# Performance work log

Hardware: AMD Instinct MI355X
Metric: run time of the kernel (lower is better)

The kernel has to match this reference:

```python
import jax, jax.numpy as jnp
import numpy as np

NUM_HEADS = 8
FOCUSING_FACTOR = 3
EPS = 1e-6


def _focus(x, f):
    # focusing: x**f, renormalized to keep the original L2 norm per token
    n = jnp.linalg.norm(x, axis=-1, keepdims=True)
    xp = x ** f
    return xp / jnp.linalg.norm(xp, axis=-1, keepdims=True) * n


def _split_heads(x, h):
    # b n (h c) -> (b h) n c
    b, n, C = x.shape
    return x.reshape(b, n, h, C // h).transpose(0, 2, 1, 3).reshape(b * h, n, C // h)


def setup_inputs() -> dict:
    key = jax.random.key(0)
    ks = jax.random.split(key, 9)
    B, Nq, Nkv, C = 8, 4096, 4096, 512
    query = jax.random.normal(ks[0], (B, Nq, C), jnp.float32)
    key_in = jax.random.normal(ks[1], (B, Nkv, C), jnp.float32)
    value = jax.random.normal(ks[2], (B, Nkv, C), jnp.float32)
    Wq = jax.random.normal(ks[3], (C, C), jnp.float32) * 0.02
    Wk = jax.random.normal(ks[4], (C, C), jnp.float32) * 0.02
    Wv = jax.random.normal(ks[5], (C, C), jnp.float32) * 0.02
    Wp = jax.random.normal(ks[6], (C, C), jnp.float32) * 0.02
    bp = jnp.zeros((C,), jnp.float32)
    scale = jax.random.normal(ks[7], (1, 1, C), jnp.float32) * 0.02
    return {"query": query, "key_in": key_in, "value": value,
            "Wq": Wq, "Wk": Wk, "Wv": Wv, "Wp": Wp, "bp": bp,
            "scale": scale, "H": 64, "W": 64}


def reference(query, key_in, value, Wq, Wk, Wv, Wp, bp, scale, H, W):
    B, N, C = query.shape
    h = NUM_HEADS
    # projections (qkv_bias=False)
    q = jax.nn.relu(query @ Wq) + EPS
    k = jax.nn.relu(key_in @ Wk) + EPS
    v = value @ Wv
    s = jax.nn.softplus(scale)  # [1,1,C]
    q = q / s
    k = k / s
    q = _focus(q, FOCUSING_FACTOR)
    k = _focus(k, FOCUSING_FACTOR)
    q = _split_heads(q, h)  # [(B h), N, c]
    k = _split_heads(k, h)
    v = _split_heads(v, h)
    # z-normalizer: 1 / (q . sum_j k_j)
    z = 1.0 / (jnp.einsum('bic,bc->bi', q, k.sum(axis=1)) + EPS)
    # O(n) kv-aggregation path (i*j*(c+d) > c*d*(i+j) for these shapes)
    kv = jnp.einsum('bjc,bjd->bcd', k, v)
    x = jnp.einsum('bic,bcd,bi->bid', q, kv, z)
    # (b h) n c -> b n (h c)
    x = x.reshape(B, h, N, C // h).transpose(0, 2, 1, 3).reshape(B, N, C)
    # note: dwc(v) feature_map in the original is dead code (never added to x)
    return x @ Wp + bp
```

## Files before the change

### kernel.cpp

```cpp
#include <hip/hip_runtime.h>
#include <hip/hip_bf16.h>
#include <math.h>

typedef __attribute__((ext_vector_type(8))) short short8;
typedef __attribute__((ext_vector_type(4))) float f32x4;

#define MFMA16x16x32(A,B,C) __builtin_amdgcn_mfma_f32_16x16x32_bf16((A),(B),(C),0,0,0)

__device__ __forceinline__ short f2b(float x) {
  __hip_bfloat16 h = __float2bfloat16(x);
  short s; __builtin_memcpy(&s, &h, 2); return s;
}
__device__ __forceinline__ float b2f(short s) {
  __hip_bfloat16 h; __builtin_memcpy(&h, &s, 2); return __bfloat162float(h);
}

__global__ __launch_bounds__(256)
void prep_kernel(const float* __restrict__ Wq, const float* __restrict__ Wk,
                 const float* __restrict__ Wv, const float* __restrict__ Wp,
                 const float* __restrict__ scale,
                 short* __restrict__ wpack, float* __restrict__ spls)
{
  const int b = blockIdx.x;
  const int t = threadIdx.x;
  if (b == 64) {
    for (int i = t; i < 512; i += 256) {
      float x = scale[i];
      spls[i] = (x > 20.f) ? x : log1pf(expf(x));
    }
    return;
  }
  const float* Ws[4] = {Wq, Wk, Wv, Wp};
  const int w = b >> 4, kf16 = b & 15;
  const float* W = Ws[w];
  short* dst = wpack + (size_t)w * (512 * 512);
  __shared__ short lds[32 * 512];
  for (int i = 0; i < 64; ++i) {
    int idx = i * 256 + t;
    int r = idx >> 9, c = idx & 511;
    lds[idx] = f2b(W[(size_t)(kf16 * 32 + r) * 512 + c]);
  }
  __syncthreads();
  for (int s = 0; s < 8; ++s) {
    int slot = s * 256 + t;
    int nf = slot >> 6, l = slot & 63;
    int n = nf * 16 + (l & 15);
    int k0 = 8 * (l >> 4);
    short8 v;
#pragma unroll
    for (int jj = 0; jj < 8; ++jj) v[jj] = lds[(k0 + jj) * 512 + n];
    *(short8*)(dst + ((size_t)(kf16 * 32 + nf) * 64 + l) * 8) = v;
  }
}

template<int MODE>
__global__ __launch_bounds__(512, 2)
void proj_kernel(const void* __restrict__ Xv, const short* __restrict__ wpk,
                 const float* __restrict__ spls, short* __restrict__ outp,
                 const float* __restrict__ bp, float* __restrict__ outf)
{
  __shared__ short tile[64 * 512];
  __shared__ float pnorm[2][8][64];
  __shared__ float facs[64];
  const int t = threadIdx.x;
  const int lane = t & 63;
  const int wid = t >> 6;
  const int g = lane >> 4;
  const int cl = lane & 15;
  const int rb = blockIdx.x << 6;

  {
    const int r = t >> 3;
    const int c8 = t & 7;
    if (MODE < 3) {
      const float* src = (const float*)Xv + (size_t)(rb + r) * 512;
#pragma unroll
      for (int s = 0; s < 8; ++s) {
        int c = s * 64 + c8 * 8;
        f32x4 a0 = *(const f32x4*)(src + c);
        f32x4 a1 = *(const f32x4*)(src + c + 4);
        short8 v;
#pragma unroll
        for (int j = 0; j < 4; ++j) { v[j] = f2b(a0[j]); v[4 + j] = f2b(a1[j]); }
        int byteoff = (r * 1024 + c * 2) ^ ((r & 7) << 4);
        *(short8*)((char*)tile + byteoff) = v;
      }
    } else {
      const short* src = (const short*)Xv + (size_t)(rb + r) * 512;
#pragma unroll
      for (int s = 0; s < 8; ++s) {
        int c = s * 64 + c8 * 8;
        short8 v = *(const short8*)(src + c);
        int byteoff = (r * 1024 + c * 2) ^ ((r & 7) << 4);
        *(short8*)((char*)tile + byteoff) = v;
      }
    }
  }
  __syncthreads();

  f32x4 zero4 = {0.f, 0.f, 0.f, 0.f};
  f32x4 acc[4][4];
#pragma unroll
  for (int rf = 0; rf < 4; ++rf)
#pragma unroll
    for (int cf = 0; cf < 4; ++cf) acc[rf][cf] = zero4;

  const short8* wp8 = (const short8*)wpk;

  short8 bcur[4], bnxt[4];
#pragma unroll
  for (int cf = 0; cf < 4; ++cf)
    bcur[cf] = wp8[((size_t)(wid * 4 + cf)) * 64 + lane];

  for (int kf = 0; kf < 16; ++kf) {
    if (kf < 15) {
#pragma unroll
      for (int cf = 0; cf < 4; ++cf)
        bnxt[cf] = wp8[((size_t)((kf + 1) * 32 + wid * 4 + cf)) * 64 + lane];
    }
    short8 af[4];
#pragma unroll
    for (int rf = 0; rf < 4; ++rf) {
      int row = rf * 16 + cl;
      int byteoff = (row * 1024 + (kf * 32 + 8 * g) * 2) ^ ((row & 7) << 4);
      af[rf] = *(const short8*)((const char*)tile + byteoff);
    }
#pragma unroll
    for (int rf = 0; rf < 4; ++rf)
#pragma unroll
      for (int cf = 0; cf < 4; ++cf)
        acc[rf][cf] = MFMA16x16x32(af[rf], bcur[cf], acc[rf][cf]);
    if (kf < 15) {
#pragma unroll
      for (int cf = 0; cf < 4; ++cf) bcur[cf] = bnxt[cf];
    }
  }

  if (MODE == 3) {
#pragma unroll
    for (int rf = 0; rf < 4; ++rf)
#pragma unroll
      for (int cf = 0; cf < 4; ++cf) {
        int c = wid * 64 + cf * 16 + cl;
        float bv = bp[c];
#pragma unroll
        for (int j = 0; j < 4; ++j)
          outf[(size_t)(rb + rf * 16 + 4 * g + j) * 512 + c] = acc[rf][cf][j] + bv;
      }
    return;
  }

  if (MODE < 2) {
    float sp_inv[4];
#pragma unroll
    for (int cf = 0; cf < 4; ++cf) sp_inv[cf] = 1.f / spls[wid * 64 + cf * 16 + cl];
    float p2[4][4], p6[4][4];
#pragma unroll
    for (int rf = 0; rf < 4; ++rf)
#pragma unroll
      for (int j = 0; j < 4; ++j) { p2[rf][j] = 0.f; p6[rf][j] = 0.f; }
#pragma unroll
    for (int rf = 0; rf < 4; ++rf)
#pragma unroll
      for (int cf = 0; cf < 4; ++cf)
#pragma unroll
        for (int j = 0; j < 4; ++j) {
          float v = acc[rf][cf][j];
          v = fmaxf(v, 0.f) + 1e-6f;
          v *= sp_inv[cf];
          acc[rf][cf][j] = v;
          float v2 = v * v;
          p2[rf][j] += v2;
          p6[rf][j] += v2 * v2 * v2;
        }
#pragma unroll
    for (int m = 1; m < 16; m <<= 1) {
#pragma unroll
      for (int rf = 0; rf < 4; ++rf)
#pragma unroll
        for (int j = 0; j < 4; ++j) {
          p2[rf][j] += __shfl_xor(p2[rf][j], m, 64);
          p6[rf][j] += __shfl_xor(p6[rf][j], m, 64);
        }
    }
    if (cl == 0) {
#pragma unroll
      for (int rf = 0; rf < 4; ++rf)
#pragma unroll
        for (int j = 0; j < 4; ++j) {
          pnorm[0][wid][rf * 16 + 4 * g + j] = p2[rf][j];
          pnorm[1][wid][rf * 16 + 4 * g + j] = p6[rf][j];
        }
    }
    __syncthreads();
    if (t < 64) {
      float a = 0.f, b = 0.f;
#pragma unroll
      for (int w = 0; w < 8; ++w) { a += pnorm[0][w][t]; b += pnorm[1][w][t]; }
      facs[t] = sqrtf(a / b);
    }
    __syncthreads();
    float fac[4][4];
#pragma unroll
    for (int rf = 0; rf < 4; ++rf)
#pragma unroll
      for (int j = 0; j < 4; ++j) fac[rf][j] = facs[rf * 16 + 4 * g + j];
#pragma unroll
    for (int rf = 0; rf < 4; ++rf)
#pragma unroll
      for (int cf = 0; cf < 4; ++cf)
#pragma unroll
        for (int j = 0; j < 4; ++j) {
          float v = acc[rf][cf][j];
          float o = v * v * v * fac[rf][j];
          int r = rf * 16 + 4 * g + j;
          int c = wid * 64 + cf * 16 + cl;
          int byteoff = (r * 1024 + c * 2) ^ ((r & 7) << 4);
          *(short*)((char*)tile + byteoff) = f2b(o);
        }
  } else {
    __syncthreads();
#pragma unroll
    for (int rf = 0; rf < 4; ++rf)
#pragma unroll
      for (int cf = 0; cf < 4; ++cf)
#pragma unroll
        for (int j = 0; j < 4; ++j) {
          int r = rf * 16 + 4 * g + j;
          int c = wid * 64 + cf * 16 + cl;
          int byteoff = (r * 1024 + c * 2) ^ ((r & 7) << 4);
          *(short*)((char*)tile + byteoff) = f2b(acc[rf][cf][j]);
        }
  }
  __syncthreads();

  if (MODE == 0) {
    const int r = t >> 3;
    const int c8 = t & 7;
#pragma unroll
    for (int s = 0; s < 8; ++s) {
      int ci = c8 + 8 * s;
      int byteoff = (r * 1024 + ci * 16) ^ ((r & 7) << 4);
      short8 v = *(const short8*)((const char*)tile + byteoff);
      *(short8*)(outp + (size_t)(rb + r) * 512 + ci * 8) = v;
    }
  } else {
    const int l = lane;
    const int batch = rb >> 12;
    const int jf_base = (rb & 4095) >> 5;
#pragma unroll
    for (int s = 0; s < 8; ++s) {
      int fidx = wid * 8 + s;
      int jf = fidx >> 5;
      int cf = fidx & 31;
      int c = cf * 16 + (l & 15);
      int j0 = jf * 32 + 8 * (l >> 4);
      short8 v;
#pragma unroll
      for (int jj = 0; jj < 8; ++jj) {
        int j = j0 + jj;
        int byteoff = (j * 1024 + c * 2) ^ ((j & 7) << 4);
        v[jj] = *(const short*)((const char*)tile + byteoff);
      }
      int bh = batch * 8 + (cf >> 2);
      int cfh = cf & 3;
      int jfg = jf_base + jf;
      *(short8*)(outp + (((size_t)(bh * 128 + jfg) * 4 + cfh) * 64 + l) * 8) = v;
    }
  }
}

__global__ __launch_bounds__(256)
void kv_kernel(const short* __restrict__ kpack, const short* __restrict__ vpack,
               float* __restrict__ pKV, float* __restrict__ pKS)
{
  __shared__ float red[4][64 * 64];
  __shared__ float ksacc[64];
  const int t = threadIdx.x;
  const int lane = t & 63;
  const int w = t >> 6;
  const int g = lane >> 4;
  const int cl = lane & 15;
  const int bh = blockIdx.x >> 3;
  const int sp = blockIdx.x & 7;
  if (t < 64) ksacc[t] = 0.f;
  __syncthreads();

  f32x4 zero4 = {0.f, 0.f, 0.f, 0.f};
  f32x4 acc[4][4];
#pragma unroll
  for (int df = 0; df < 4; ++df)
#pragma unroll
    for (int cf = 0; cf < 4; ++cf) acc[df][cf] = zero4;
  float ks[4] = {0.f, 0.f, 0.f, 0.f};
  const short8* kp = (const short8*)kpack;
  const short8* vp = (const short8*)vpack;

#pragma unroll
  for (int i = 0; i < 4; ++i) {
    int jfg = sp * 16 + w * 4 + i;
    size_t base = ((size_t)bh * 128 + jfg) * 4 * 64;
    short8 afr[4], bfr[4];
#pragma unroll
    for (int f = 0; f < 4; ++f) {
      afr[f] = vp[base + (size_t)f * 64 + lane];
      bfr[f] = kp[base + (size_t)f * 64 + lane];
    }
#pragma unroll
    for (int cf = 0; cf < 4; ++cf) {
      float s = 0.f;
#pragma unroll
      for (int jj = 0; jj < 8; ++jj) s += b2f(bfr[cf][jj]);
      ks[cf] += s;
    }
#pragma unroll
    for (int df = 0; df < 4; ++df)
#pragma unroll
      for (int cf = 0; cf < 4; ++cf)
        acc[df][cf] = MFMA16x16x32(afr[df], bfr[cf], acc[df][cf]);
  }

#pragma unroll
  for (int cf = 0; cf < 4; ++cf) {
    ks[cf] += __shfl_xor(ks[cf], 16, 64);
    ks[cf] += __shfl_xor(ks[cf], 32, 64);
  }
  if (lane < 16) {
#pragma unroll
    for (int cf = 0; cf < 4; ++cf) atomicAdd(&ksacc[cf * 16 + lane], ks[cf]);
  }

#pragma unroll
  for (int df = 0; df < 4; ++df)
#pragma unroll
    for (int cf = 0; cf < 4; ++cf)
#pragma unroll
      for (int j = 0; j < 4; ++j)
        red[w][(df * 16 + 4 * g + j) * 64 + cf * 16 + cl] = acc[df][cf][j];
  __syncthreads();

  float* dkv = pKV + (size_t)blockIdx.x * 4096;
  for (int i = t; i < 4096; i += 256)
    dkv[i] = red[0][i] + red[1][i] + red[2][i] + red[3][i];
  if (t < 64) pKS[(size_t)blockIdx.x * 64 + t] = ksacc[t];
}

__global__ __launch_bounds__(256)
void kv_reduce(const float* __restrict__ pKV, const float* __restrict__ pKS,
               short* __restrict__ kvT, float* __restrict__ ksum)
{
  const int bh = blockIdx.x;
  const int t = threadIdx.x;
  for (int i = t; i < 4096; i += 256) {
    float s = 0.f;
#pragma unroll
    for (int sp = 0; sp < 8; ++sp) s += pKV[(size_t)(bh * 8 + sp) * 4096 + i];
    kvT[(size_t)bh * 4096 + i] = f2b(s);
  }
  if (t < 64) {
    float s = 0.f;
#pragma unroll
    for (int sp = 0; sp < 8; ++sp) s += pKS[(size_t)(bh * 8 + sp) * 64 + t];
    ksum[bh * 64 + t] = s;
  }
}

__global__ __launch_bounds__(512)
void x_kernel(const short* __restrict__ qf, const short* __restrict__ kvT,
              const float* __restrict__ ksum, short* __restrict__ xout)
{
  __shared__ short xt[64 * 512];
  __shared__ float ksb[512];
  __shared__ float zb[64 * 8];
  const int t = threadIdx.x;
  const int lane = t & 63;
  const int wid = t >> 6;
  const int wr = wid >> 1;
  const int wc = wid & 1;
  const int g = lane >> 4;
  const int cl = lane & 15;
  const int rb = blockIdx.x << 6;
  const int batch = rb >> 12;

  ksb[t] = ksum[batch * 512 + t];
  __syncthreads();

  {
    int r = t >> 3, h = t & 7;
    const short8* qrow = (const short8*)(qf + (size_t)(rb + r) * 512 + h * 64);
    float d = 0.f;
#pragma unroll
    for (int c8 = 0; c8 < 8; ++c8) {
      short8 qv = qrow[c8];
#pragma unroll
      for (int jj = 0; jj < 8; ++jj) d += b2f(qv[jj]) * ksb[h * 64 + c8 * 8 + jj];
    }
    zb[r * 8 + h] = 1.f / (d + 1e-6f);
  }
  __syncthreads();

  f32x4 zero4 = {0.f, 0.f, 0.f, 0.f};
  f32x4 xacc[16];
#pragma unroll
  for (int i = 0; i < 16; ++i) xacc[i] = zero4;

  const short8* q8 = (const short8*)qf;
  const size_t qrowbase = (size_t)(rb + wr * 16 + cl) * 64;
#pragma unroll
  for (int hh = 0; hh < 4; ++hh) {
    int h = wc * 4 + hh;
    short8 af0 = q8[qrowbase + h * 8 + g];
    short8 af1 = q8[qrowbase + h * 8 + 4 + g];
    const short8* kv8 = (const short8*)kvT + ((size_t)(batch * 8 + h)) * 512;
#pragma unroll
    for (int nfl = 0; nfl < 4; ++nfl) {
      short8 b0 = kv8[(size_t)(nfl * 16 + cl) * 8 + g];
      short8 b1 = kv8[(size_t)(nfl * 16 + cl) * 8 + 4 + g];
      int nf = hh * 4 + nfl;
      xacc[nf] = MFMA16x16x32(af0, b0, xacc[nf]);
      xacc[nf] = MFMA16x16x32(af1, b1, xacc[nf]);
    }
  }
#pragma unroll
  for (int hh = 0; hh < 4; ++hh) {
    int h = wc * 4 + hh;
    float z4[4];
#pragma unroll
    for (int j = 0; j < 4; ++j) z4[j] = zb[(wr * 16 + 4 * g + j) * 8 + h];
#pragma unroll
    for (int nfl = 0; nfl < 4; ++nfl) {
      int nf = hh * 4 + nfl;
#pragma unroll
      for (int j = 0; j < 4; ++j) {
        float xv = xacc[nf][j] * z4[j];
        int r = wr * 16 + 4 * g + j;
        int c = wc * 256 + nf * 16 + cl;
        int byteoff = (r * 1024 + c * 2) ^ ((r & 7) << 4);
        *(short*)((char*)xt + byteoff) = f2b(xv);
      }
    }
  }
  __syncthreads();

  const int r = t >> 3;
  const int c8 = t & 7;
#pragma unroll
  for (int s = 0; s < 8; ++s) {
    int ci = c8 + 8 * s;
    int byteoff = (r * 1024 + ci * 16) ^ ((r & 7) << 4);
    short8 v = *(const short8*)((const char*)xt + byteoff);
    *(short8*)(xout + (size_t)(rb + r) * 512 + ci * 8) = v;
  }
}

extern "C" void kernel_launch(void* const* d_in, const int* in_sizes, int n_in,
                              void* d_out, int out_size, void* d_ws, size_t ws_size,
                              hipStream_t stream)
{
  const float* query  = (const float*)d_in[0];
  const float* key_in = (const float*)d_in[1];
  const float* value  = (const float*)d_in[2];
  const float* Wq     = (const float*)d_in[3];
  const float* Wk     = (const float*)d_in[4];
  const float* Wv     = (const float*)d_in[5];
  const float* Wp     = (const float*)d_in[6];
  const float* bp     = (const float*)d_in[7];
  const float* scale  = (const float*)d_in[8];
  float* out = (float*)d_out;

  char* ws = (char*)d_ws;
  size_t off = 0;
  auto alloc = [&](size_t bytes) -> void* {
    void* p = ws + off;
    off += (bytes + 255) & ~(size_t)255;
    return p;
  };
  float* spls  = (float*)alloc(512 * 4);
  short* wpack = (short*)alloc((size_t)4 * 512 * 512 * 2);
  short* qf    = (short*)alloc((size_t)32768 * 512 * 2);
  short* kpack = (short*)alloc((size_t)32768 * 512 * 2);
  short* vpack = (short*)alloc((size_t)32768 * 512 * 2);
  float* pKV   = (float*)alloc((size_t)512 * 4096 * 4);
  float* pKS   = (float*)alloc((size_t)512 * 64 * 4);
  short* kvT   = (short*)alloc((size_t)64 * 4096 * 2);
  float* ksum  = (float*)alloc((size_t)64 * 64 * 4);
  short* xbuf  = kpack;

  prep_kernel<<<65, 256, 0, stream>>>(Wq, Wk, Wv, Wp, scale, wpack, spls);
  proj_kernel<0><<<512, 512, 0, stream>>>(query,  wpack + (size_t)0 * 512 * 512, spls, qf,    nullptr, nullptr);
  proj_kernel<1><<<512, 512, 0, stream>>>(key_in, wpack + (size_t)1 * 512 * 512, spls, kpack, nullptr, nullptr);
  proj_kernel<2><<<512, 512, 0, stream>>>(value,  wpack + (size_t)2 * 512 * 512, spls, vpack, nullptr, nullptr);
  kv_kernel<<<512, 256, 0, stream>>>(kpack, vpack, pKV, pKS);
  kv_reduce<<<64, 256, 0, stream>>>(pKV, pKS, kvT, ksum);
  x_kernel<<<512, 512, 0, stream>>>(qf, kvT, ksum, xbuf);
  proj_kernel<3><<<512, 512, 0, stream>>>(xbuf, wpack + (size_t)3 * 512 * 512, spls, nullptr, bp, out);
}
```

Before: 210.7 us.

## Double-buffer activation tile in K-chunks to overlap global loads with MFMA

The projection kernel now stages the 64x512 activation tile in four 128-column chunks using two padded LDS buffers (272-byte row stride instead of an XOR swizzle). While MFMAs run on the current chunk, the next chunk is loaded into registers and written to the other buffer. This hides global load latency and shrinks the tile footprint. Launch bounds are raised to target four blocks per CU, which adds register pressure and one barrier per chunk. The 64 KB smem array is still declared, so the footprint reduction may not actually happen.

```diff
diff --git a/kernel.cpp b/kernel.cpp
--- a/kernel.cpp
+++ b/kernel.cpp
@@ -54,50 +54,49 @@
 }
 
 template<int MODE>
-__global__ __launch_bounds__(512, 2)
+__global__ __launch_bounds__(512, 4)
 void proj_kernel(const void* __restrict__ Xv, const short* __restrict__ wpk,
                  const float* __restrict__ spls, short* __restrict__ outp,
                  const float* __restrict__ bp, float* __restrict__ outf)
 {
-  __shared__ short tile[64 * 512];
+  __shared__ char smem[65536];
   __shared__ float pnorm[2][8][64];
   __shared__ float facs[64];
+  short* tile = (short*)smem;
   const int t = threadIdx.x;
   const int lane = t & 63;
   const int wid = t >> 6;
   const int g = lane >> 4;
   const int cl = lane & 15;
   const int rb = blockIdx.x << 6;
+  const int sr = t >> 3;
+  const int sc = t & 7;
+
+  const float* Xf = (const float*)Xv;
+  const short* Xb = (const short*)Xv;
+  const short8* wp8 = (const short8*)wpk;
 
   {
-    const int r = t >> 3;
-    const int c8 = t & 7;
+    char* dst = smem + sr * 272 + sc * 32;
     if (MODE < 3) {
-      const float* src = (const float*)Xv + (size_t)(rb + r) * 512;
-#pragma unroll
-      for (int s = 0; s < 8; ++s) {
-        int c = s * 64 + c8 * 8;
-        f32x4 a0 = *(const f32x4*)(src + c);
-        f32x4 a1 = *(const f32x4*)(src + c + 4);
-        short8 v;
-#pragma unroll
-        for (int j = 0; j < 4; ++j) { v[j] = f2b(a0[j]); v[4 + j] = f2b(a1[j]); }
-        int byteoff = (r * 1024 + c * 2) ^ ((r & 7) << 4);
-        *(short8*)((char*)tile + byteoff) = v;
-      }
+      const float* src = Xf + (size_t)(rb + sr) * 512 + sc * 16;
+      f32x4 a0 = *(const f32x4*)(src);
+      f32x4 a1 = *(const f32x4*)(src + 4);
+      f32x4 a2 = *(const f32x4*)(src + 8);
+      f32x4 a3 = *(const f32x4*)(src + 12);
+      short8 v0, v1;
+#pragma unroll
+      for (int j = 0; j < 4; ++j) {
+        v0[j] = f2b(a0[j]); v0[4 + j] = f2b(a1[j]);
+        v1[j] = f2b(a2[j]); v1[4 + j] = f2b(a3[j]);
+      }
+      *(short8*)dst = v0; *(short8*)(dst + 16) = v1;
     } else {
-      const short* src = (const short*)Xv + (size_t)(rb + r) * 512;
-#pragma unroll
-      for (int s = 0; s < 8; ++s) {
-        int c = s * 64 + c8 * 8;
-        short8 v = *(const short8*)(src + c);
-        int byteoff = (r * 1024 + c * 2) ^ ((r & 7) << 4);
-        *(short8*)((char*)tile + byteoff) = v;
-      }
-    }
-  }
-  __syncthreads();
-
+      const short* src = Xb + (size_t)(rb + sr) * 512 + sc * 16;
+      *(short8*)dst = *(const short8*)src;
+      *(short8*)(dst + 16) = *(const short8*)(src + 8);
+    }
+  }
   f32x4 zero4 = {0.f, 0.f, 0.f, 0.f};
   f32x4 acc[4][4];
 #pragma unroll
@@ -105,34 +104,65 @@
 #pragma unroll
     for (int cf = 0; cf < 4; ++cf) acc[rf][cf] = zero4;
 
-  const short8* wp8 = (const short8*)wpk;
-
   short8 bcur[4], bnxt[4];
 #pragma unroll
   for (int cf = 0; cf < 4; ++cf)
     bcur[cf] = wp8[((size_t)(wid * 4 + cf)) * 64 + lane];
-
-  for (int kf = 0; kf < 16; ++kf) {
-    if (kf < 15) {
-#pragma unroll
-      for (int cf = 0; cf < 4; ++cf)
-        bnxt[cf] = wp8[((size_t)((kf + 1) * 32 + wid * 4 + cf)) * 64 + lane];
-    }
-    short8 af[4];
-#pragma unroll
-    for (int rf = 0; rf < 4; ++rf) {
-      int row = rf * 16 + cl;
-      int byteoff = (row * 1024 + (kf * 32 + 8 * g) * 2) ^ ((row & 7) << 4);
-      af[rf] = *(const short8*)((const char*)tile + byteoff);
-    }
-#pragma unroll
-    for (int rf = 0; rf < 4; ++rf)
-#pragma unroll
-      for (int cf = 0; cf < 4; ++cf)
-        acc[rf][cf] = MFMA16x16x32(af[rf], bcur[cf], acc[rf][cf]);
-    if (kf < 15) {
-#pragma unroll
-      for (int cf = 0; cf < 4; ++cf) bcur[cf] = bnxt[cf];
+  __syncthreads();
+
+#pragma unroll
+  for (int s = 0; s < 4; ++s) {
+    char* cur = smem + (s & 1) * 17408;
+    char* nxt = smem + ((s + 1) & 1) * 17408;
+    f32x4 rA0, rA1, rA2, rA3;
+    short8 rB0, rB1;
+    if (s < 3) {
+      if (MODE < 3) {
+        const float* src = Xf + (size_t)(rb + sr) * 512 + (s + 1) * 128 + sc * 16;
+        rA0 = *(const f32x4*)(src);
+        rA1 = *(const f32x4*)(src + 4);
+        rA2 = *(const f32x4*)(src + 8);
+        rA3 = *(const f32x4*)(src + 12);
+      } else {
+        const short* src = Xb + (size_t)(rb + sr) * 512 + (s + 1) * 128 + sc * 16;
+        rB0 = *(const short8*)src;
+        rB1 = *(const short8*)(src + 8);
+      }
+    }
+#pragma unroll
+    for (int kfl = 0; kfl < 4; ++kfl) {
+      const int kf = s * 4 + kfl;
+      if (kf < 15) {
+#pragma unroll
+        for (int cf = 0; cf < 4; ++cf)
+          bnxt[cf] = wp8[((size_t)((kf + 1) * 32 + wid * 4 + cf)) * 64 + lane];
+      }
+      short8 af[4];
+#pragma unroll
+      for (int rf = 0; rf < 4; ++rf)
+        af[rf] = *(const short8*)(cur + (rf * 16 + cl) * 272 + kfl * 64 + 16 * g);
+#pragma unroll
+      for (int rf = 0; rf < 4; ++rf)
+#pragma unroll
+        for (int cf = 0; cf < 4; ++cf)
+          acc[rf][cf] = MFMA16x16x32(af[rf], bcur[cf], acc[rf][cf]);
+      if (kf < 15) {
+#pragma unroll
+        for (int cf = 0; cf < 4; ++cf) bcur[cf] = bnxt[cf];
+      }
+    }
+    if (s < 3) {
+      char* dst = nxt + sr * 272 + sc * 32;
+      short8 v0, v1;
+      if (MODE < 3) {
+#pragma unroll
+        for (int j = 0; j < 4; ++j) {
+          v0[j] = f2b(rA0[j]); v0[4 + j] = f2b(rA1[j]);
+          v1[j] = f2b(rA2[j]); v1[4 + j] = f2b(rA3[j]);
+        }
+      } else { v0 = rB0; v1 = rB1; }
+      *(short8*)dst = v0; *(short8*)(dst + 16) = v1;
+      __syncthreads();
     }
   }
 
```

Measured after the change: 263.7 us. 25.2% more time.
